# Kernel optimization log

Hardware: AMD Instinct MI355X
Metric: run time of the kernel (lower is better)

Reference implementation:

```python
import jax, jax.numpy as jnp
import numpy as np

IN_FEATURES = 4096
OUT_FEATURES = 11008


def setup_inputs() -> dict:
    key = jax.random.key(0)
    k1, k2, k3, k4 = jax.random.split(key, 4)
    x = jax.random.normal(k1, (2, 2048, IN_FEATURES), dtype=jnp.float32)
    # two signed int4 values packed per byte: low nibble = even k, high nibble = odd k
    w_packed = jax.random.randint(k2, (OUT_FEATURES, IN_FEATURES // 2), 0, 256, dtype=jnp.int32)
    # rowwise dequant scales (positive, roughly max|w|/7 scale)
    w_scales = jax.random.uniform(k3, (OUT_FEATURES,), dtype=jnp.float32, minval=0.001, maxval=0.02)
    bias = jax.random.normal(k4, (OUT_FEATURES,), dtype=jnp.float32)
    return {"x": x, "w_packed": w_packed, "w_scales": w_scales, "bias": bias}


def _dequantize(w_packed, w_scales):
    # unpack two int4 nibbles per byte
    low = w_packed & 0xF            # [O, K//2]
    high = (w_packed >> 4) & 0xF    # [O, K//2]
    q = jnp.stack([low, high], axis=-1).reshape(w_packed.shape[0], -1)  # [O, K]
    q = jnp.where(q >= 8, q - 16, q)  # sign-extend int4 to [-8, 7]
    return q.astype(w_scales.dtype) * w_scales[:, None]  # [O, K]


def reference(x, w_packed, w_scales, bias):
    w = _dequantize(w_packed, w_scales)               # [O, K] fp32
    y = jnp.einsum('bsk,ok->bso', x, w)               # GEMM
    return y + bias
```

## Files before the change

### kernel.cpp

```cpp
#include <hip/hip_runtime.h>
#include <hip/hip_bf16.h>
#include <stdint.h>

#define M_DIM 4096
#define K_DIM 4096
#define N_DIM 11008
#define KP    2048

#define BK2   64
#define NKT   (K_DIM/BK2)
#define NTM2  (M_DIM/256)
#define NTN2  (N_DIM/256)
#define NBLK2 (NTM2*NTN2)
#define HT_BYTES 8192

#define BM 128
#define BN 128
#define BK 64
#define NTM (M_DIM/BM)
#define NTN (N_DIM/BN)
#define NBLK (NTM*NTN)

typedef __attribute__((ext_vector_type(8)))  short bf16x8;
typedef __attribute__((ext_vector_type(4)))  float f32x4;
typedef __attribute__((ext_vector_type(4)))  int   i32x4;
typedef __attribute__((ext_vector_type(16))) int   i32x16;
typedef __attribute__((ext_vector_type(16))) char  c8x16;
typedef __attribute__((ext_vector_type(8)))  unsigned short u16x8;

typedef const void __attribute__((address_space(1)))* gas_ptr;
typedef void __attribute__((address_space(3)))* las_ptr;

__device__ __forceinline__ void async_copy16(void* lds, const void* g) {
  __builtin_amdgcn_global_load_lds((gas_ptr)g, (las_ptr)lds, 16, 0, 0);
}

__device__ __forceinline__ unsigned short f2bf_rne(float f) {
  uint32_t u = __builtin_bit_cast(uint32_t, f);
  u += 0x7FFFu + ((u >> 16) & 1u);
  return (unsigned short)(u >> 16);
}
__device__ __forceinline__ unsigned short i2bf(int v) {
  float f = (float)v;
  return (unsigned short)(__builtin_bit_cast(uint32_t, f) >> 16);
}
__device__ __forceinline__ int sx4(int b, int which) {
  return ((int)((uint32_t)b << (28 - 4 * which))) >> 28;
}


__global__ __launch_bounds__(256) void quant_x_fused(const float* __restrict__ x,
                                                     char* __restrict__ wsA,
                                                     float* __restrict__ xs) {
  const int grow = blockIdx.x;
  const int tid  = threadIdx.x;
  const float4* src = (const float4*)(x + (size_t)grow * K_DIM + tid * 16);
  float4 v0 = src[0], v1 = src[1], v2 = src[2], v3 = src[3];
  float vv[16] = { v0.x, v0.y, v0.z, v0.w, v1.x, v1.y, v1.z, v1.w,
                   v2.x, v2.y, v2.z, v2.w, v3.x, v3.y, v3.z, v3.w };
  float m = 0.f;
#pragma unroll
  for (int j = 0; j < 16; ++j) m = fmaxf(m, fabsf(vv[j]));
#pragma unroll
  for (int off = 32; off >= 1; off >>= 1) m = fmaxf(m, __shfl_xor(m, off));
  __shared__ float sm[4];
  if ((tid & 63) == 0) sm[tid >> 6] = m;
  __syncthreads();
  m = fmaxf(fmaxf(sm[0], sm[1]), fmaxf(sm[2], sm[3]));
  const float rs = (m > 0.f) ? 127.0f / m : 0.f;
  if (tid == 0) xs[grow] = m * (1.0f / 127.0f);
  c8x16 q;
#pragma unroll
  for (int j = 0; j < 16; ++j) q[j] = (char)__float2int_rn(vv[j] * rs);
  const int kt = tid >> 2, e = tid & 3;
  const int tm = grow >> 8, wi = grow & 255, h = wi >> 7, r = wi & 127;
  const int c = (r >> 5) * 128 + (e >> 1) * 64 + (e & 1) * 32 + (r & 31);
  *(c8x16*)(wsA + ((size_t)(tm * NKT + kt) * 2 + h) * HT_BYTES + c * 16) = q;
}

__global__ __launch_bounds__(256) void deq_w_i8(const int* __restrict__ wp,
                                                char* __restrict__ wsB) {
  const int total = NTN2 * NKT * 2 * 512;
  for (int i = blockIdx.x * blockDim.x + threadIdx.x; i < total;
       i += gridDim.x * blockDim.x) {
    int rc  = i & 511;
    int h   = (i >> 9) & 1;
    int kt  = (i >> 10) & 63;
    int tn  = i >> 16;
    int row = rc >> 2, e = rc & 3;
    const int4* src = (const int4*)(wp + (size_t)(tn * 256 + h * 128 + row) * KP + kt * 32 + e * 8);
    int4 a = src[0], b = src[1];
    c8x16 q;
    q[0]  = (char)sx4(a.x, 0); q[1]  = (char)sx4(a.x, 1);
    q[2]  = (char)sx4(a.y, 0); q[3]  = (char)sx4(a.y, 1);
    q[4]  = (char)sx4(a.z, 0); q[5]  = (char)sx4(a.z, 1);
    q[6]  = (char)sx4(a.w, 0); q[7]  = (char)sx4(a.w, 1);
    q[8]  = (char)sx4(b.x, 0); q[9]  = (char)sx4(b.x, 1);
    q[10] = (char)sx4(b.y, 0); q[11] = (char)sx4(b.y, 1);
    q[12] = (char)sx4(b.z, 0); q[13] = (char)sx4(b.z, 1);
    q[14] = (char)sx4(b.w, 0); q[15] = (char)sx4(b.w, 1);
    int c = (row >> 5) * 128 + (e >> 1) * 64 + (e & 1) * 32 + (row & 31);
    *(c8x16*)(wsB + (size_t)(i >> 9) * HT_BYTES + c * 16) = q;
  }
}

__global__ __launch_bounds__(512, 2)
void qgemm8i(const char* __restrict__ wsA, const char* __restrict__ wsB,
             const float* __restrict__ xs,
             const float* __restrict__ scales, const float* __restrict__ bias,
             float* __restrict__ out) {
  __shared__ __align__(16) char smem[65536];

  const int tid  = threadIdx.x;
  const int lane = tid & 63, wid = tid >> 6;
  const int wr = wid >> 2, wc = wid & 3;
  const int l31 = lane & 31, kg = lane >> 5;

  int bid = blockIdx.x;
  int id  = (bid & 7) * (NBLK2 / 8) + (bid >> 3);
  int tm  = id & (NTM2 - 1), tn = id >> 4;

  const char* gA = wsA + (size_t)tm * (NKT * 2) * HT_BYTES;
  const char* gB = wsB + (size_t)tn * (NKT * 2) * HT_BYTES;

  const char* baseA = smem + wr * HT_BYTES + lane * 16;
  const char* baseB = smem + 16384 + (wc >> 1) * HT_BYTES + lane * 16;

#define STAGE(ldsoff, src) \
    async_copy16(smem + (ldsoff) + wid * 1024, (src) + wid * 1024 + lane * 16)
#define STAGE_A(buf, h, kt) STAGE((buf) * 32768 + (h) * HT_BYTES, gA + ((kt) * 2 + (h)) * HT_BYTES)
#define STAGE_B(buf, h, kt) STAGE((buf) * 32768 + 16384 + (h) * HT_BYTES, gB + ((kt) * 2 + (h)) * HT_BYTES)

  i32x16 acc[4][2] = {};
  i32x4  aS0[2][2], aS1[2][2];
  i32x4  bS0[2], bS1[2];

#define LDA_SET(dst, buf, sel) do { \
    _Pragma("unroll") for (int i = 0; i < 2; ++i) \
    _Pragma("unroll") for (int ks = 0; ks < 2; ++ks) \
      dst[i][ks] = *(const i32x4*)(baseA + (buf) * 32768 + ((sel) * 2 + i) * 2048 + ks * 1024); \
  } while (0)
#define LDB_SET(dst, buf, bn) do { \
    _Pragma("unroll") for (int ks = 0; ks < 2; ++ks) \
      dst[ks] = *(const i32x4*)(baseB + (buf) * 32768 + ((wc & 1) * 2 + (bn)) * 2048 + ks * 1024); \
  } while (0)
#define MMQ(aS, bS, sel, bn) do { \
    _Pragma("unroll") for (int ks = 0; ks < 2; ++ks) \
    _Pragma("unroll") for (int i = 0; i < 2; ++i) \
      acc[(sel) * 2 + i][bn] = __builtin_amdgcn_mfma_i32_32x32x32_i8( \
          aS[i][ks], bS[ks], acc[(sel) * 2 + i][bn], 0, 0, 0); \
  } while (0)

#define PH_BAR __builtin_amdgcn_s_barrier()
#define LGKM0 asm volatile("s_waitcnt lgkmcnt(0)" ::: "memory")
#define VMC2  asm volatile("s_waitcnt vmcnt(2)" ::: "memory")
#define PRIO1 __builtin_amdgcn_s_setprio(1)
#define PRIO0 __builtin_amdgcn_s_setprio(0)

  STAGE_B(0, 0, 0); STAGE_B(0, 1, 0);
  STAGE_A(0, 0, 0); STAGE_A(0, 1, 0);
  STAGE_B(1, 0, 1); STAGE_B(1, 1, 1);
  VMC2;
  PH_BAR;
  LDA_SET(aS0, 0, 0); LDB_SET(bS0, 0, 0); LDB_SET(bS1, 0, 1);

  for (int t = 0; t < NKT / 2; ++t) {
    const int k1 = 2 * t + 1;
    const int k2 = (2 * t + 2 < NKT) ? 2 * t + 2 : NKT - 1;
    const int k3 = (2 * t + 3 < NKT) ? 2 * t + 3 : NKT - 1;

    LGKM0;
    PRIO1; MMQ(aS0, bS0, 0, 0); MMQ(aS0, bS1, 0, 1); PRIO0;
    STAGE_A(1, 0, k1); STAGE_A(1, 1, k1);
    LDA_SET(aS1, 0, 1);
    PH_BAR;
    LGKM0;
    PRIO1; MMQ(aS1, bS1, 1, 1); MMQ(aS1, bS0, 1, 0); PRIO0;
    STAGE_B(0, 0, k2); STAGE_B(0, 1, k2);
    VMC2;
    LDA_SET(aS0, 1, 0); LDB_SET(bS0, 1, 0); LDB_SET(bS1, 1, 1);
    PH_BAR;
    LGKM0;
    PRIO1; MMQ(aS0, bS0, 0, 0); MMQ(aS0, bS1, 0, 1); PRIO0;
    STAGE_A(0, 0, k2); STAGE_A(0, 1, k2);
    LDA_SET(aS1, 1, 1);
    PH_BAR;
    LGKM0;
    PRIO1; MMQ(aS1, bS1, 1, 1); MMQ(aS1, bS0, 1, 0); PRIO0;
    STAGE_B(1, 0, k3); STAGE_B(1, 1, k3);
    VMC2;
    LDA_SET(aS0, 0, 0); LDB_SET(bS0, 0, 0); LDB_SET(bS1, 0, 1);
    PH_BAR;
  }

  const int m0 = tm * 256, n0 = tn * 256;
#pragma unroll
  for (int ni = 0; ni < 2; ++ni) {
    const int o = n0 + wc * 64 + ni * 32 + l31;
    const float sw = scales[o];
    const float b = bias[o];
#pragma unroll
    for (int mi = 0; mi < 4; ++mi) {
      const int mrb = m0 + wr * 128 + mi * 32 + kg * 4;
#pragma unroll
      for (int r = 0; r < 16; ++r) {
        const int mr = mrb + (r & 3) + 8 * (r >> 2);
        const float y = (float)acc[mi][ni][r] * xs[mr] * sw + b;
        __builtin_nontemporal_store(y, out + (size_t)mr * N_DIM + o);
      }
    }
  }
#undef STAGE
#undef STAGE_A
#undef STAGE_B
#undef LDA_SET
#undef LDB_SET
#undef MMQ
#undef PH_BAR
#undef LGKM0
#undef VMC2
#undef PRIO1
#undef PRIO0
}

__global__ __launch_bounds__(256) void cvt_x_kernel(const float* __restrict__ x,
                                                    unsigned short* __restrict__ xb) {
  const int n4 = M_DIM * K_DIM / 4;
  int i = blockIdx.x * blockDim.x + threadIdx.x;
  const int stride = gridDim.x * blockDim.x;
  for (; i < n4; i += stride) {
    float4 v = ((const float4*)x)[i];
    ushort4 r;
    r.x = f2bf_rne(v.x); r.y = f2bf_rne(v.y);
    r.z = f2bf_rne(v.z); r.w = f2bf_rne(v.w);
    ((ushort4*)xb)[i] = r;
  }
}

template <int MODE>
__global__ __launch_bounds__(256)
void qgemm_kernel(const float* __restrict__ x, const unsigned short* __restrict__ xb,
                  const int* __restrict__ wp,
                  const float* __restrict__ scales, const float* __restrict__ bias,
                  float* __restrict__ out) {
  __shared__ __align__(16) unsigned short As[BM * BK];
  __shared__ __align__(16) unsigned short Bs[BN * BK];
  const int tid  = threadIdx.x;
  const int lane = tid & 63;
  const int wid  = tid >> 6;
  int bid = blockIdx.x;
  int swzb = (bid & 7) * (NBLK / 8) + (bid >> 3);
  const int tm = swzb & (NTM - 1);
  const int tn = swzb >> 5;
  const int m0 = tm * BM, n0 = tn * BN;
  const int wr = wid >> 1, wc = wid & 1;
  const int fr = lane & 15;
  const int fg = lane >> 4;
  f32x4 acc[4][4] = {};

  for (int kt = 0; kt < K_DIM / BK; ++kt) {
    int4   breg[4];
    float4 areg[8];
#pragma unroll
    for (int p = 0; p < 4; ++p) {
      int fl = p * 256 + tid;
      int row = fl >> 3, u = fl & 7;
      breg[p] = *(const int4*)(wp + (size_t)(n0 + row) * KP + kt * (BK / 2) + u * 4);
    }
    if constexpr (MODE == 2) {
#pragma unroll
      for (int p = 0; p < 8; ++p) {
        int fl = p * 256 + tid;
        int row = fl >> 4, u = fl & 15;
        areg[p] = *(const float4*)(x + (size_t)(m0 + row) * K_DIM + kt * BK + u * 4);
      }
    }
    __syncthreads();
    if constexpr (MODE == 1) {
#pragma unroll
      for (int p = 0; p < 4; ++p) {
        int t16 = p * 256 + tid;
        int row = t16 >> 3, u = t16 & 7;
        const unsigned short* g = xb + (size_t)(m0 + row) * K_DIM + kt * BK + u * 8;
        async_copy16((char*)As + (p * 256 + wid * 64) * 16, g);
      }
    } else {
#pragma unroll
      for (int p = 0; p < 8; ++p) {
        int fl = p * 256 + tid;
        int row = fl >> 4, u = fl & 15;
        ushort4 r;
        r.x = f2bf_rne(areg[p].x); r.y = f2bf_rne(areg[p].y);
        r.z = f2bf_rne(areg[p].z); r.w = f2bf_rne(areg[p].w);
        *(ushort4*)((char*)As + row * 128 + u * 8) = r;
      }
    }
#pragma unroll
    for (int p = 0; p < 4; ++p) {
      int fl = p * 256 + tid;
      int row = fl >> 3, u = fl & 7;
      int4 b = breg[p];
      u16x8 r;
      r[0] = i2bf(sx4(b.x, 0)); r[1] = i2bf(sx4(b.x, 1));
      r[2] = i2bf(sx4(b.y, 0)); r[3] = i2bf(sx4(b.y, 1));
      r[4] = i2bf(sx4(b.z, 0)); r[5] = i2bf(sx4(b.z, 1));
      r[6] = i2bf(sx4(b.w, 0)); r[7] = i2bf(sx4(b.w, 1));
      *(u16x8*)((char*)Bs + row * 128 + u * 16) = r;
    }
    __syncthreads();
#pragma unroll
    for (int kk = 0; kk < 2; ++kk) {
      const int kb = kk * 64 + fg * 16;
      bf16x8 af[4], bfv[4];
#pragma unroll
      for (int mi = 0; mi < 4; ++mi) {
        int row = wr * 64 + mi * 16 + fr;
        af[mi] = *(const bf16x8*)((const char*)As + row * 128 + kb);
      }
#pragma unroll
      for (int ni = 0; ni < 4; ++ni) {
        int row = wc * 64 + ni * 16 + fr;
        bfv[ni] = *(const bf16x8*)((const char*)Bs + row * 128 + kb);
      }
#pragma unroll
      for (int mi = 0; mi < 4; ++mi)
#pragma unroll
        for (int ni = 0; ni < 4; ++ni)
          acc[mi][ni] = __builtin_amdgcn_mfma_f32_16x16x32_bf16(af[mi], bfv[ni], acc[mi][ni], 0, 0, 0);
    }
  }
#pragma unroll
  for (int ni = 0; ni < 4; ++ni) {
    const int o = n0 + wc * 64 + ni * 16 + fr;
    const float s = scales[o];
    const float b = bias[o];
#pragma unroll
    for (int mi = 0; mi < 4; ++mi) {
      const int mr = m0 + wr * 64 + mi * 16 + fg * 4;
#pragma unroll
      for (int r = 0; r < 4; ++r)
        out[(size_t)(mr + r) * N_DIM + o] = acc[mi][ni][r] * s + b;
    }
  }
}

extern "C" void kernel_launch(void* const* d_in, const int* in_sizes, int n_in,
                              void* d_out, int out_size, void* d_ws, size_t ws_size,
                              hipStream_t stream) {
  const float* x  = (const float*)d_in[0];
  const int*   wp = (const int*)d_in[1];
  const float* sc = (const float*)d_in[2];
  const float* bs = (const float*)d_in[3];
  float* out = (float*)d_out;

  const size_t a_bytes  = (size_t)NTM2 * NKT * 2 * HT_BYTES;
  const size_t b_bytes  = (size_t)NTN2 * NKT * 2 * HT_BYTES;
  const size_t xs_bytes = (size_t)M_DIM * 4;
  char*  wsA = (char*)d_ws;
  char*  wsB = (char*)d_ws + a_bytes;
  float* xs  = (float*)((char*)d_ws + a_bytes + b_bytes);

  if (ws_size >= a_bytes + b_bytes + xs_bytes) {
    quant_x_fused<<<M_DIM, 256, 0, stream>>>(x, wsA, xs);
    deq_w_i8<<<2048, 256, 0, stream>>>(wp, wsB);
    qgemm8i<<<NBLK2, 512, 0, stream>>>(wsA, wsB, xs, sc, bs, out);
  } else if (ws_size >= (size_t)M_DIM * K_DIM * 2) {
    cvt_x_kernel<<<2048, 256, 0, stream>>>(x, (unsigned short*)d_ws);
    qgemm_kernel<1><<<NBLK, 256, 0, stream>>>(x, (unsigned short*)d_ws, wp, sc, bs, out);
  } else {
    qgemm_kernel<2><<<NBLK, 256, 0, stream>>>(x, (unsigned short*)d_ws, wp, sc, bs, out);
  }
}
```

Baseline: 247.3 us.

## Shrink int8 GEMM block tile to 128x256 for higher occupancy

The int8 MFMA GEMM block tile drops from 256x256 to 128x256. Each wave now holds a 64x64 accumulator instead of 128x64, LDS shrinks to 48KB per block, and launch bounds ask for 4 blocks per CU. The grid doubles, which should reduce tail-wave quantization and allow more resident waves to hide latency. The LDS-load and async-staging order inside the k-loop is also reshuffled around the barriers. The cost is lower data reuse per block: more global and LDS traffic per MFMA, and A fragments are loaded right before use with less time to overlap.

```diff
diff --git a/kernel.cpp b/kernel.cpp
--- a/kernel.cpp
+++ b/kernel.cpp
@@ -11,8 +11,9 @@
 #define NKT   (K_DIM/BK2)
 #define NTM2  (M_DIM/256)
 #define NTN2  (N_DIM/256)
-#define NBLK2 (NTM2*NTN2)
 #define HT_BYTES 8192
+#define NTM128 (M_DIM/128)
+#define NBLK128 (NTM128*NTN2)
 
 #define BM 128
 #define BN 128
@@ -104,12 +105,12 @@
   }
 }
 
-__global__ __launch_bounds__(512, 2)
-void qgemm8i(const char* __restrict__ wsA, const char* __restrict__ wsB,
-             const float* __restrict__ xs,
-             const float* __restrict__ scales, const float* __restrict__ bias,
-             float* __restrict__ out) {
-  __shared__ __align__(16) char smem[65536];
+__global__ __launch_bounds__(512, 4)
+void qgemm128(const char* __restrict__ wsA, const char* __restrict__ wsB,
+              const float* __restrict__ xs,
+              const float* __restrict__ scales, const float* __restrict__ bias,
+              float* __restrict__ out) {
+  __shared__ __align__(16) char smem[49152];
 
   const int tid  = threadIdx.x;
   const int lane = tid & 63, wid = tid >> 6;
@@ -117,38 +118,35 @@
   const int l31 = lane & 31, kg = lane >> 5;
 
   int bid = blockIdx.x;
-  int id  = (bid & 7) * (NBLK2 / 8) + (bid >> 3);
-  int tm  = id & (NTM2 - 1), tn = id >> 4;
-
-  const char* gA = wsA + (size_t)tm * (NKT * 2) * HT_BYTES;
+  int id  = (bid & 7) * (NBLK128 / 8) + (bid >> 3);
+  int tm  = id & (NTM128 - 1), tn = id >> 5;
+
+  const char* gA = wsA + ((size_t)(tm >> 1) * (NKT * 2) + (tm & 1)) * HT_BYTES;
   const char* gB = wsB + (size_t)tn * (NKT * 2) * HT_BYTES;
 
-  const char* baseA = smem + wr * HT_BYTES + lane * 16;
-  const char* baseB = smem + 16384 + (wc >> 1) * HT_BYTES + lane * 16;
+  const char* baseA = smem + lane * 16;
+  const char* baseB = smem + 8192 + (wc >> 1) * HT_BYTES + lane * 16;
 
 #define STAGE(ldsoff, src) \
     async_copy16(smem + (ldsoff) + wid * 1024, (src) + wid * 1024 + lane * 16)
-#define STAGE_A(buf, h, kt) STAGE((buf) * 32768 + (h) * HT_BYTES, gA + ((kt) * 2 + (h)) * HT_BYTES)
-#define STAGE_B(buf, h, kt) STAGE((buf) * 32768 + 16384 + (h) * HT_BYTES, gB + ((kt) * 2 + (h)) * HT_BYTES)
-
-  i32x16 acc[4][2] = {};
-  i32x4  aS0[2][2], aS1[2][2];
+#define STAGE_A(buf, kt)    STAGE((buf) * 24576, gA + (size_t)(kt) * 2 * HT_BYTES)
+#define STAGE_B(buf, h, kt) STAGE((buf) * 24576 + 8192 + (h) * 8192, gB + ((kt) * 2 + (h)) * HT_BYTES)
+
+  i32x16 acc[2][2] = {};
+  i32x4  aS0[2], aS1[2];
   i32x4  bS0[2], bS1[2];
 
-#define LDA_SET(dst, buf, sel) do { \
-    _Pragma("unroll") for (int i = 0; i < 2; ++i) \
+#define LDA_SET(dst, buf, msub) do { \
     _Pragma("unroll") for (int ks = 0; ks < 2; ++ks) \
-      dst[i][ks] = *(const i32x4*)(baseA + (buf) * 32768 + ((sel) * 2 + i) * 2048 + ks * 1024); \
+      dst[ks] = *(const i32x4*)(baseA + (buf) * 24576 + ((wr) * 2 + (msub)) * 2048 + ks * 1024); \
   } while (0)
 #define LDB_SET(dst, buf, bn) do { \
     _Pragma("unroll") for (int ks = 0; ks < 2; ++ks) \
-      dst[ks] = *(const i32x4*)(baseB + (buf) * 32768 + ((wc & 1) * 2 + (bn)) * 2048 + ks * 1024); \
+      dst[ks] = *(const i32x4*)(baseB + (buf) * 24576 + ((wc & 1) * 2 + (bn)) * 2048 + ks * 1024); \
   } while (0)
-#define MMQ(aS, bS, sel, bn) do { \
+#define MMQ(aS, bS, mi, bn) do { \
     _Pragma("unroll") for (int ks = 0; ks < 2; ++ks) \
-    _Pragma("unroll") for (int i = 0; i < 2; ++i) \
-      acc[(sel) * 2 + i][bn] = __builtin_amdgcn_mfma_i32_32x32x32_i8( \
-          aS[i][ks], bS[ks], acc[(sel) * 2 + i][bn], 0, 0, 0); \
+      acc[mi][bn] = __builtin_amdgcn_mfma_i32_32x32x32_i8(aS[ks], bS[ks], acc[mi][bn], 0, 0, 0); \
   } while (0)
 
 #define PH_BAR __builtin_amdgcn_s_barrier()
@@ -158,50 +156,49 @@
 #define PRIO0 __builtin_amdgcn_s_setprio(0)
 
   STAGE_B(0, 0, 0); STAGE_B(0, 1, 0);
-  STAGE_A(0, 0, 0); STAGE_A(0, 1, 0);
+  STAGE_A(0, 0);
   STAGE_B(1, 0, 1); STAGE_B(1, 1, 1);
   VMC2;
   PH_BAR;
-  LDA_SET(aS0, 0, 0); LDB_SET(bS0, 0, 0); LDB_SET(bS1, 0, 1);
 
   for (int t = 0; t < NKT / 2; ++t) {
     const int k1 = 2 * t + 1;
     const int k2 = (2 * t + 2 < NKT) ? 2 * t + 2 : NKT - 1;
     const int k3 = (2 * t + 3 < NKT) ? 2 * t + 3 : NKT - 1;
 
+    LDA_SET(aS0, 0, 0); LDB_SET(bS0, 0, 0); LDB_SET(bS1, 0, 1);
+    STAGE_A(1, k1);
     LGKM0;
     PRIO1; MMQ(aS0, bS0, 0, 0); MMQ(aS0, bS1, 0, 1); PRIO0;
-    STAGE_A(1, 0, k1); STAGE_A(1, 1, k1);
+    PH_BAR;
     LDA_SET(aS1, 0, 1);
-    PH_BAR;
+    STAGE_B(0, 0, k2); STAGE_B(0, 1, k2);
     LGKM0;
     PRIO1; MMQ(aS1, bS1, 1, 1); MMQ(aS1, bS0, 1, 0); PRIO0;
-    STAGE_B(0, 0, k2); STAGE_B(0, 1, k2);
     VMC2;
+    PH_BAR;
     LDA_SET(aS0, 1, 0); LDB_SET(bS0, 1, 0); LDB_SET(bS1, 1, 1);
-    PH_BAR;
+    STAGE_A(0, k2);
     LGKM0;
     PRIO1; MMQ(aS0, bS0, 0, 0); MMQ(aS0, bS1, 0, 1); PRIO0;
-    STAGE_A(0, 0, k2); STAGE_A(0, 1, k2);
+    PH_BAR;
     LDA_SET(aS1, 1, 1);
-    PH_BAR;
+    STAGE_B(1, 0, k3); STAGE_B(1, 1, k3);
     LGKM0;
     PRIO1; MMQ(aS1, bS1, 1, 1); MMQ(aS1, bS0, 1, 0); PRIO0;
-    STAGE_B(1, 0, k3); STAGE_B(1, 1, k3);
     VMC2;
-    LDA_SET(aS0, 0, 0); LDB_SET(bS0, 0, 0); LDB_SET(bS1, 0, 1);
     PH_BAR;
   }
 
-  const int m0 = tm * 256, n0 = tn * 256;
+  const int m0 = tm * 128, n0 = tn * 256;
 #pragma unroll
   for (int ni = 0; ni < 2; ++ni) {
     const int o = n0 + wc * 64 + ni * 32 + l31;
     const float sw = scales[o];
     const float b = bias[o];
 #pragma unroll
-    for (int mi = 0; mi < 4; ++mi) {
-      const int mrb = m0 + wr * 128 + mi * 32 + kg * 4;
+    for (int mi = 0; mi < 2; ++mi) {
+      const int mrb = m0 + wr * 64 + mi * 32 + kg * 4;
 #pragma unroll
       for (int r = 0; r < 16; ++r) {
         const int mr = mrb + (r & 3) + 8 * (r >> 2);
@@ -363,7 +360,7 @@
   if (ws_size >= a_bytes + b_bytes + xs_bytes) {
     quant_x_fused<<<M_DIM, 256, 0, stream>>>(x, wsA, xs);
     deq_w_i8<<<2048, 256, 0, stream>>>(wp, wsB);
-    qgemm8i<<<NBLK2, 512, 0, stream>>>(wsA, wsB, xs, sc, bs, out);
+    qgemm128<<<NBLK128, 512, 0, stream>>>(wsA, wsB, xs, sc, bs, out);
   } else if (ws_size >= (size_t)M_DIM * K_DIM * 2) {
     cvt_x_kernel<<<2048, 256, 0, stream>>>(x, (unsigned short*)d_ws);
     qgemm_kernel<1><<<NBLK, 256, 0, stream>>>(x, (unsigned short*)d_ws, wp, sc, bs, out);
```

Measured after the change: 263.7 us. +6.7%, slower.
